# Kernel optimization log

Measured on AMD Instinct MI355X. Metric: run time of the kernel, lower is better.

## Reference

```python
import jax, jax.numpy as jnp
import numpy as np

C = 16          # in_channels // 4
EXP = 16        # expand_rate
SHIFTS = [1, 3, 5, 7]
BN_EPS = 1e-5

# fixed directional-difference kernels (non-trainable in the torch module)
_tmp1 = np.array([[[-1,0,0],[0,1,0],[0,0,0]],
                  [[0,-1,0],[0,1,0],[0,0,0]],
                  [[0,0,-1],[0,1,0],[0,0,0]],
                  [[0,0,0],[-1,1,0],[0,0,0]]], dtype=np.float32).reshape(4,1,3,3)
_tmp2 = _tmp1[:, :, ::-1, ::-1].copy()
K1 = jnp.asarray(np.tile(np.concatenate([_tmp1, _tmp2], 0), (C,1,1,1)))  # [8C,1,3,3]
K2 = jnp.asarray(np.tile(np.concatenate([_tmp2, _tmp1], 0), (C,1,1,1)))  # [8C,1,3,3]

def conv(x, w, groups=1, dilation=1, bias=None):
    out = jax.lax.conv_general_dilated(
        x, w, window_strides=(1,1), padding='SAME',
        rhs_dilation=(dilation, dilation),
        dimension_numbers=('NCHW','OIHW','NCHW'),
        feature_group_count=groups)
    if bias is not None:
        out = out + bias[None, :, None, None]
    return out

def setup_inputs() -> dict:
    key = jax.random.key(0)
    ks = jax.random.split(key, 20)
    B, Cin, H, W = 4, 64, 256, 256
    inp = {
        'cen': jax.random.normal(ks[0], (B, Cin, H, W), jnp.float32),
        'mas': jax.random.normal(ks[1], (B, 1, H, W), jnp.float32),
        'w_in': jax.random.normal(ks[2], (C, Cin, 1, 1), jnp.float32) * 0.1,
        'b_in': jax.random.normal(ks[3], (C,), jnp.float32) * 0.1,
        'w_c0': jax.random.normal(ks[4], (C, C, 1, 1), jnp.float32) * 0.1,
        'b_c0': jax.random.normal(ks[5], (C,), jnp.float32) * 0.1,
        'w_c1': jax.random.normal(ks[6], (C, C, 3, 3), jnp.float32) * 0.1,
        'b_c1': jax.random.normal(ks[7], (C,), jnp.float32) * 0.1,
        'w_c2': jax.random.normal(ks[8], (C, C, 5, 5), jnp.float32) * 0.05,
        'b_c2': jax.random.normal(ks[9], (C,), jnp.float32) * 0.1,
        'w_c3': jax.random.normal(ks[10], (C, C, 7, 7), jnp.float32) * 0.05,
        'b_c3': jax.random.normal(ks[11], (C,), jnp.float32) * 0.1,
        'scales1': jax.random.normal(ks[12], (4,), jnp.float32) * 0.1,
        'scales2': jax.random.normal(ks[13], (C * EXP, 8, 1, 1), jnp.float32) * 0.1,
        'scales3': jax.random.normal(ks[14], (C, EXP, 1, 1), jnp.float32) * 0.1,
        'w_base': jax.random.normal(ks[15], (C, C, 3, 3), jnp.float32) * 0.1,
        'bn_gamma': jnp.ones((C,), jnp.float32),
        'bn_beta': jnp.zeros((C,), jnp.float32),
        'bn_mean': jnp.zeros((C,), jnp.float32),
        'bn_var': jnp.ones((C,), jnp.float32),
        'w_out': jax.random.normal(ks[16], (1, C, 1, 1), jnp.float32) * 0.1,
        'b_out': jax.random.normal(ks[17], (1,), jnp.float32) * 0.1,
    }
    return inp

def reference(cen, mas, w_in, b_in, w_c0, b_c0, w_c1, b_c1, w_c2, b_c2, w_c3, b_c3,
              scales1, scales2, scales3, w_base, bn_gamma, bn_beta, bn_mean, bn_var,
              w_out, b_out):
    x = conv(cen, w_in, bias=b_in)                      # [B,C,H,W]
    k3 = jax.nn.softmax(scales2, axis=1)                # [8C*2? no: [C*EXP,8,1,1]
    k4 = jax.nn.softmax(scales3, axis=1)                # [C,EXP,1,1]
    conv_ws = [(w_c0, b_c0), (w_c1, b_c1), (w_c2, b_c2), (w_c3, b_c3)]
    outs = []
    for (wc, bc), shift in zip(conv_ws, SHIFTS):
        c = conv(x, wc, bias=bc)                        # [B,C,H,W]
        o1 = conv(c, K1, groups=C, dilation=shift)      # [B,8C,H,W]
        o2 = conv(c, K2, groups=C, dilation=shift)
        o1 = conv(o1, k3, groups=C)                     # [B,C*EXP,H,W]
        o2 = conv(o2, k3, groups=C)
        o = jnp.sort(o1 * o2, axis=2)                   # sort along H
        o = jax.nn.silu(o)
        o = conv(o, k4, groups=C)                       # [B,C,H,W]
        outs.append(o)
    outs = jnp.stack(outs, axis=-1)                     # [B,C,H,W,4]
    outs = jnp.max(outs, axis=-1) + jnp.mean(outs, axis=-1)
    # out_conv = BaseConv(3x3 conv -> BN(eval) -> SiLU) then 1x1 conv to 1 ch
    h = conv(outs, w_base)
    h = (h - bn_mean[None, :, None, None]) * jax.lax.rsqrt(bn_var + BN_EPS)[None, :, None, None]
    h = h * bn_gamma[None, :, None, None] + bn_beta[None, :, None, None]
    h = jax.nn.silu(h)
    h = conv(h, w_out, bias=b_out)
    out_mask = jax.nn.sigmoid(h)                        # [B,1,H,W]
    s = jax.nn.softmax(scales1, axis=-1)
    m = jax.nn.sigmoid(mas)
    return cen * (out_mask * m * s[0] + m * s[1] + s[2] * out_mask + s[3])
```

## Files before the change

kernel.cpp:

```cpp
#include <hip/hip_runtime.h>

#define HW 65536

constexpr int OFF_X    = 0;
constexpr int OFF_CT   = 4194304;
constexpr int OFF_MAX  = 8388608;
constexpr int OFF_SUM  = 12582912;
constexpr int OFF_MASK = 16777216;
constexpr int P_K3  = 17039360;
constexpr int P_K3S = P_K3  + 2048;
constexpr int P_K4  = P_K3S + 2048;
constexpr int P_S1  = P_K4  + 256;
constexpr int P_BNS = P_S1  + 4;
constexpr int P_BNB = P_BNS + 16;
constexpr int P_WRI = P_BNB + 16;
constexpr int P_WR0 = P_WRI + 1024;
constexpr int P_WR1 = P_WR0 + 256;
constexpr int P_WR2 = P_WR1 + 2304;
constexpr int P_WR3 = P_WR2 + 6400;
constexpr int P_WRB = P_WR3 + 12544;
constexpr int P_K3H  = P_WRB + 2304;
constexpr int P_K3SH = P_K3H + 1024;

typedef _Float16 hv2 __attribute__((ext_vector_type(2)));

__device__ __forceinline__ int h2i(hv2 v) { return __builtin_bit_cast(int, v); }
__device__ __forceinline__ hv2 i2h(int v) { return __builtin_bit_cast(hv2, v); }

__device__ __forceinline__ hv2 pkrtz(float a, float b) {
  return __builtin_bit_cast(hv2, __builtin_amdgcn_cvt_pkrtz(a, b));
}

__device__ __forceinline__ hv2 pk_fma_n(hv2 a, hv2 b, hv2 c) {
#if __has_builtin(__builtin_elementwise_fma)
  return __builtin_elementwise_fma(a, b, c);
#else
  return a * b + c;
#endif
}

__device__ __forceinline__ hv2 pkmin(hv2 a, hv2 b) {
  hv2 d; asm("v_pk_min_f16 %0, %1, %2" : "=v"(d) : "v"(a), "v"(b)); return d;
}
__device__ __forceinline__ hv2 pkmax(hv2 a, hv2 b) {
  hv2 d; asm("v_pk_max_f16 %0, %1, %2" : "=v"(d) : "v"(a), "v"(b)); return d;
}
__device__ __forceinline__ hv2 pkmul(hv2 a, hv2 b) {
  hv2 d; asm("v_pk_mul_f16 %0, %1, %2" : "=v"(d) : "v"(a), "v"(b)); return d;
}
__device__ __forceinline__ hv2 pkfma(hv2 a, hv2 b, hv2 c) {
  hv2 d; asm("v_pk_fma_f16 %0, %1, %2, %3" : "=v"(d) : "v"(a), "v"(b), "v"(c)); return d;
}

__device__ __forceinline__ hv2 sel32(bool c, hv2 a, hv2 b) {
  return i2h(c ? h2i(a) : h2i(b));
}

template <int LMASK>
__device__ __forceinline__ int lane_xor_i(int x) {
  if constexpr (LMASK < 32) {
    return __builtin_amdgcn_ds_swizzle(x, (LMASK << 10) | 0x1F);
  } else {
    return __shfl_xor(x, LMASK, 64);
  }
}

__device__ __forceinline__ float sigmoid_fast(float x) {
  return __fdividef(1.0f, 1.0f + __expf(-x));
}

__global__ void k_prep(const float* __restrict__ w_in, const float* __restrict__ w_c0,
                       const float* __restrict__ w_c1, const float* __restrict__ w_c2,
                       const float* __restrict__ w_c3, const float* __restrict__ w_base,
                       const float* __restrict__ scales1, const float* __restrict__ scales2,
                       const float* __restrict__ scales3, const float* __restrict__ bn_gamma,
                       const float* __restrict__ bn_beta, const float* __restrict__ bn_mean,
                       const float* __restrict__ bn_var, float* __restrict__ ws) {
  int tid = threadIdx.x;
  {
    const float* srow = scales2 + tid * 8;
    float v[8]; float mx = -1e30f;
    for (int j = 0; j < 8; j++) { v[j] = srow[j]; mx = fmaxf(mx, v[j]); }
    float s = 0.f;
    for (int j = 0; j < 8; j++) { v[j] = __expf(v[j] - mx); s += v[j]; }
    float inv = 1.0f / s;
    for (int j = 0; j < 8; j++) ws[P_K3 + tid * 8 + j] = v[j] * inv;
    for (int j = 0; j < 8; j++) ws[P_K3S + tid * 8 + j] = v[(j + 4) & 7] * inv;
  }
  if (tid < 16) {
    const float* srow = scales3 + tid * 16;
    float v[16]; float mx = -1e30f;
    for (int e = 0; e < 16; e++) { v[e] = srow[e]; mx = fmaxf(mx, v[e]); }
    float s = 0.f;
    for (int e = 0; e < 16; e++) { v[e] = __expf(v[e] - mx); s += v[e]; }
    float inv = 1.0f / s;
    for (int e = 0; e < 16; e++) ws[P_K4 + tid * 16 + e] = v[e] * inv;
  }
  if (tid == 0) {
    float v[4]; float mx = -1e30f;
    for (int i = 0; i < 4; i++) { v[i] = scales1[i]; mx = fmaxf(mx, v[i]); }
    float s = 0.f;
    for (int i = 0; i < 4; i++) { v[i] = __expf(v[i] - mx); s += v[i]; }
    for (int i = 0; i < 4; i++) ws[P_S1 + i] = v[i] / s;
  }
  if (tid < 16) {
    float rs = rsqrtf(bn_var[tid] + 1e-5f);
    float sc = bn_gamma[tid] * rs;
    ws[P_BNS + tid] = sc;
    ws[P_BNB + tid] = bn_beta[tid] - bn_mean[tid] * sc;
  }
  for (int i = tid; i < 1024; i += 256) { int ci = i >> 4, co = i & 15; ws[P_WRI + i] = w_in[co * 64 + ci]; }
  {
    uint32_t* w0 = (uint32_t*)(ws + P_WR0);
    for (int i = tid; i < 128; i += 256) {
      int cp = i & 7, ci = i >> 3;
      hv2 wv;
      wv.x = (_Float16)w_c0[(2 * cp) * 16 + ci];
      wv.y = (_Float16)w_c0[(2 * cp + 1) * 16 + ci];
      w0[ci * 8 + cp] = __builtin_bit_cast(uint32_t, wv);
    }
    uint32_t* w1 = (uint32_t*)(ws + P_WR1);
    for (int i = tid; i < 1152; i += 256) {
      int cp = i & 7; int r = i >> 3; int kw = r % 3; r /= 3; int kh = r % 3; int ci = r / 3;
      hv2 wv;
      wv.x = (_Float16)w_c1[((2 * cp) * 16 + ci) * 9 + kh * 3 + kw];
      wv.y = (_Float16)w_c1[((2 * cp + 1) * 16 + ci) * 9 + kh * 3 + kw];
      w1[((ci * 3 + kh) * 3 + kw) * 8 + cp] = __builtin_bit_cast(uint32_t, wv);
    }
    uint32_t* w2 = (uint32_t*)(ws + P_WR2);
    for (int i = tid; i < 3200; i += 256) {
      int cp = i & 7; int r = i >> 3; int kw = r % 5; r /= 5; int kh = r % 5; int ci = r / 5;
      hv2 wv;
      wv.x = (_Float16)w_c2[((2 * cp) * 16 + ci) * 25 + kh * 5 + kw];
      wv.y = (_Float16)w_c2[((2 * cp + 1) * 16 + ci) * 25 + kh * 5 + kw];
      w2[((ci * 5 + kh) * 5 + kw) * 8 + cp] = __builtin_bit_cast(uint32_t, wv);
    }
    uint32_t* w3 = (uint32_t*)(ws + P_WR3);
    for (int i = tid; i < 6272; i += 256) {
      int cp = i & 7; int r = i >> 3; int kw = r % 7; r /= 7; int kh = r % 7; int ci = r / 7;
      hv2 wv;
      wv.x = (_Float16)w_c3[((2 * cp) * 16 + ci) * 49 + kh * 7 + kw];
      wv.y = (_Float16)w_c3[((2 * cp + 1) * 16 + ci) * 49 + kh * 7 + kw];
      w3[((ci * 7 + kh) * 7 + kw) * 8 + cp] = __builtin_bit_cast(uint32_t, wv);
    }
  }
  for (int i = tid; i < 2304; i += 256) {
    int co = i & 15; int r = i >> 4; int kh = r % 3; r /= 3; int kw = r % 3; int g = r / 3;
    ws[P_WRB + i] = w_base[((co * 16 + g) * 3 + kh) * 3 + kw];
  }
  __syncthreads();
  uint32_t* k3h  = (uint32_t*)(ws + P_K3H);
  uint32_t* k3sh = (uint32_t*)(ws + P_K3SH);
  for (int i = tid; i < 1024; i += 256) {
    int g = i >> 6, p = (i >> 3) & 7, j = i & 7;
    hv2 wv, wvs;
    wv.x  = (_Float16)ws[P_K3 + g * 128 + (2 * p) * 8 + j];
    wv.y  = (_Float16)ws[P_K3 + g * 128 + (2 * p + 1) * 8 + j];
    wvs.x = (_Float16)ws[P_K3S + g * 128 + (2 * p) * 8 + j];
    wvs.y = (_Float16)ws[P_K3S + g * 128 + (2 * p + 1) * 8 + j];
    k3h[i]  = __builtin_bit_cast(uint32_t, wv);
    k3sh[i] = __builtin_bit_cast(uint32_t, wvs);
  }
}

__global__ __launch_bounds__(256) void k_in(const float* __restrict__ cen,
                                            const float* __restrict__ b_in,
                                            const float* __restrict__ ws,
                                            float* __restrict__ xT) {
  __shared__ float ldst[16 * 16 * 17];
  int tid = threadIdx.x;
  int b = blockIdx.z;
  int hbase = blockIdx.y * 16, wbase = blockIdx.x * 16;
  int ty = tid >> 4, tx = tid & 15;
  const float* wri = ws + P_WRI;
  float acc[16];
#pragma unroll
  for (int co = 0; co < 16; co++) acc[co] = b_in[co];
  const float* cp = cen + b * 64 * HW + (hbase + ty) * 256 + wbase + tx;
#pragma unroll 4
  for (int ci = 0; ci < 64; ci++) {
    float v = cp[ci * HW];
#pragma unroll
    for (int co = 0; co < 16; co++) acc[co] = fmaf(wri[ci * 16 + co], v, acc[co]);
  }
#pragma unroll
  for (int co = 0; co < 16; co++) ldst[(co * 16 + tx) * 17 + ty] = acc[co];
  __syncthreads();
  int wy = tid >> 4, hx = tid & 15;
#pragma unroll
  for (int ci = 0; ci < 16; ci++) {
    xT[((b * 16 + ci) << 16) + (wbase + wy) * 256 + hbase + hx] =
        ldst[(ci * 16 + wy) * 17 + hx];
  }
}

template <int KS>
__global__ __launch_bounds__(256) void k_conv(const float* __restrict__ xT,
                                              const float* __restrict__ bias,
                                              const uint32_t* __restrict__ wrh,
                                              float* __restrict__ cT) {
  constexpr int P = KS / 2;
  const int tid = threadIdx.x;
  const int lane = tid & 63;
  const int wv = (blockIdx.x << 2) + (tid >> 6);
  const int hseg = wv & 3;
  const int w = (wv >> 2) & 255;
  const int b = wv >> 10;
  const int hbase = hseg << 6;
  const float* xb = xT + ((b * 16) << 16);

  hv2 acc[8];
#pragma unroll
  for (int cp = 0; cp < 8; cp++) {
    hv2 bv;
    bv.x = (_Float16)bias[2 * cp];
    bv.y = (_Float16)bias[2 * cp + 1];
    acc[cp] = bv;
  }

  for (int ci = 0; ci < 16; ci++) {
#pragma unroll
    for (int kw = 0; kw < KS; kw++) {
      const int wc = w + kw - P;
      if ((unsigned)wc >= 256u) continue;
      const float* col = xb + (ci << 16) + (wc << 8);
      const int h0 = hbase + lane - P;
      float v0 = ((unsigned)h0 < 256u) ? col[h0] : 0.0f;
      float v1 = 0.0f;
      if (P > 0) {
        const int h1 = hbase + 64 - P + lane;
        v1 = (lane < 2 * P && (unsigned)h1 < 256u) ? col[h1] : 0.0f;
      }
#pragma unroll
      for (int kh = 0; kh < KS; kh++) {
        float tv;
        if (P == 0) {
          tv = v0;
        } else {
          const int s = lane + kh;
          float t0 = __shfl(v0, s & 63, 64);
          float t1 = __shfl(v1, (s - 64) & 63, 64);
          tv = (s < 64) ? t0 : t1;
        }
        const hv2 tp = pkrtz(tv, tv);
        const uint32_t* wp = wrh + ((ci * KS + kh) * KS + kw) * 8;
#pragma unroll
        for (int cp = 0; cp < 8; cp++)
          acc[cp] = pk_fma_n(i2h((int)wp[cp]), tp, acc[cp]);
      }
    }
  }
  float* o = cT + ((b * 16) << 16) + (w << 8) + hbase + lane;
#pragma unroll
  for (int cp = 0; cp < 8; cp++) {
    o[(2 * cp) << 16] = (float)acc[cp].x;
    o[(2 * cp + 1) << 16] = (float)acc[cp].y;
  }
}

__device__ __forceinline__ void ce_pair_h(hv2& a, hv2& b, bool up) {
  hv2 lo = pkmin(a, b);
  hv2 hi = pkmax(a, b);
  a = sel32(up, lo, hi);
  b = sel32(up, hi, lo);
}

template <int SIZE, int DIST>
__device__ __forceinline__ void stage_x_h(hv2 v[4], int i0) {
  const bool keepmin = (((i0 & DIST) == 0) == ((i0 & SIZE) == 0));
#pragma unroll
  for (int r = 0; r < 4; r++) {
    hv2 pv = i2h(lane_xor_i<(DIST >> 2)>(h2i(v[r])));
    v[r] = sel32(keepmin, pkmin(v[r], pv), pkmax(v[r], pv));
  }
}

template <int SIZE>
__device__ __forceinline__ void stage_d21_h(hv2 v[4], int i0) {
  bool up = ((i0 & SIZE) == 0);
  ce_pair_h(v[0], v[2], up); ce_pair_h(v[1], v[3], up);
  ce_pair_h(v[0], v[1], up); ce_pair_h(v[2], v[3], up);
}

__device__ __forceinline__ void sort256h(hv2 v[4], int lane) {
  int i0 = lane << 2;
  ce_pair_h(v[0], v[1], true); ce_pair_h(v[2], v[3], false);
  stage_d21_h<4>(v, i0);
  stage_x_h<8, 4>(v, i0); stage_d21_h<8>(v, i0);
  stage_x_h<16, 8>(v, i0); stage_x_h<16, 4>(v, i0); stage_d21_h<16>(v, i0);
  stage_x_h<32, 16>(v, i0); stage_x_h<32, 8>(v, i0); stage_x_h<32, 4>(v, i0); stage_d21_h<32>(v, i0);
  stage_x_h<64, 32>(v, i0); stage_x_h<64, 16>(v, i0); stage_x_h<64, 8>(v, i0); stage_x_h<64, 4>(v, i0); stage_d21_h<64>(v, i0);
  stage_x_h<128, 64>(v, i0); stage_x_h<128, 32>(v, i0); stage_x_h<128, 16>(v, i0); stage_x_h<128, 8>(v, i0); stage_x_h<128, 4>(v, i0); stage_d21_h<128>(v, i0);
  stage_x_h<256, 128>(v, i0); stage_x_h<256, 64>(v, i0); stage_x_h<256, 32>(v, i0); stage_x_h<256, 16>(v, i0); stage_x_h<256, 8>(v, i0); stage_x_h<256, 4>(v, i0); stage_d21_h<256>(v, i0);
}

template <int DIL>
__global__ __launch_bounds__(256) void k_branch(const float* __restrict__ cT,
                                                const float* __restrict__ ws,
                                                float* __restrict__ maxb,
                                                float* __restrict__ sumb,
                                                int initFlag) {
  const int tid = threadIdx.x;
  const int lane = tid & 63;
  const int wid = __builtin_amdgcn_readfirstlane(tid >> 6);
  const int wv = (blockIdx.x << 2) + wid;
  const int w = wv & 255;
  const int g = (wv >> 8) & 15;
  const int b = wv >> 12;
  const float* base = cT + ((b * 16 + g) << 16);

  float vals[3][3][4];
#pragma unroll
  for (int wi = 0; wi < 3; ++wi) {
    const int wc = w + (wi - 1) * DIL;
    const bool wok = ((unsigned)wc < 256u);
    const float* col = base + (wok ? wc : 0) * 256;
#pragma unroll
    for (int si = 0; si < 3; ++si) {
#pragma unroll
      for (int r = 0; r < 4; ++r) {
        const int h = lane + (r << 6) + (si - 1) * DIL;
        const bool ok = wok && ((unsigned)h < 256u);
        vals[wi][si][r] = ok ? col[h] : 0.0f;
      }
    }
  }
  hv2 ddh[8][4];
#pragma unroll
  for (int r = 0; r < 4; ++r) {
    const float c0 = vals[1][1][r];
    float d0 = c0 - vals[0][0][r];
    float d1 = c0 - vals[1][0][r];
    float d2 = c0 - vals[2][0][r];
    float d3 = c0 - vals[0][1][r];
    float d4 = c0 - vals[2][2][r];
    float d5 = c0 - vals[1][2][r];
    float d6 = c0 - vals[0][2][r];
    float d7 = c0 - vals[2][1][r];
    ddh[0][r] = pkrtz(d0, d0);
    ddh[1][r] = pkrtz(d1, d1);
    ddh[2][r] = pkrtz(d2, d2);
    ddh[3][r] = pkrtz(d3, d3);
    ddh[4][r] = pkrtz(d4, d4);
    ddh[5][r] = pkrtz(d5, d5);
    ddh[6][r] = pkrtz(d6, d6);
    ddh[7][r] = pkrtz(d7, d7);
  }
  float out[4] = {0.f, 0.f, 0.f, 0.f};
  const uint32_t* k3h  = (const uint32_t*)(ws + P_K3H)  + g * 64;
  const uint32_t* k3sh = (const uint32_t*)(ws + P_K3SH) + g * 64;
  const float* k4p = ws + P_K4 + g * 16;
#pragma unroll 1
  for (int p = 0; p < 8; ++p) {
    hv2 t[4];
    hv2 wk3[8], wk3s[8];
#pragma unroll
    for (int j = 0; j < 8; ++j) {
      wk3[j]  = i2h((int)k3h[p * 8 + j]);
      wk3s[j] = i2h((int)k3sh[p * 8 + j]);
    }
#pragma unroll
    for (int r = 0; r < 4; ++r) {
      hv2 o1 = pkmul(wk3[0], ddh[0][r]);
      hv2 o2 = pkmul(wk3s[0], ddh[0][r]);
#pragma unroll
      for (int j = 1; j < 8; ++j) {
        o1 = pkfma(wk3[j], ddh[j][r], o1);
        o2 = pkfma(wk3s[j], ddh[j][r], o2);
      }
      t[r] = pkmul(o1, o2);
    }
    sort256h(t, lane);
    const float k4a = k4p[2 * p], k4b = k4p[2 * p + 1];
#pragma unroll
    for (int r = 0; r < 4; ++r) {
      const float va = (float)t[r].x;
      const float vb = (float)t[r].y;
      out[r] = fmaf(k4a, va * sigmoid_fast(va), out[r]);
      out[r] = fmaf(k4b, vb * sigmoid_fast(vb), out[r]);
    }
  }
  const int obase = (((b * 16 + g) << 8) + w) * 256 + (lane << 2);
  float4 o4 = make_float4(out[0], out[1], out[2], out[3]);
  float4* mp = (float4*)(maxb + obase);
  float4* sp = (float4*)(sumb + obase);
  if (initFlag) {
    *mp = o4;
    *sp = o4;
  } else {
    float4 m = *mp;
    m.x = fmaxf(m.x, o4.x); m.y = fmaxf(m.y, o4.y);
    m.z = fmaxf(m.z, o4.z); m.w = fmaxf(m.w, o4.w);
    *mp = m;
    float4 s = *sp;
    s.x += o4.x; s.y += o4.y; s.z += o4.z; s.w += o4.w;
    *sp = s;
  }
}

__global__ __launch_bounds__(256) void k_tail(const float* __restrict__ maxb,
                                              const float* __restrict__ sumb,
                                              const float* __restrict__ ws,
                                              float* __restrict__ mask,
                                              const float* __restrict__ w_out,
                                              const float* __restrict__ b_out) {
  __shared__ float lds[16 * 18 * 18];
  __shared__ float ldsm[256];
  int tid = threadIdx.x;
  int b = blockIdx.z;
  int wbase = blockIdx.x * 16, hbase = blockIdx.y * 16;
  const float* mb = maxb + (b * 16) * HW;
  const float* sb = sumb + (b * 16) * HW;
  for (int i = tid; i < 16 * 18 * 18; i += 256) {
    int g = i / 324; int r = i % 324; int xx = r / 18, yy = r % 18;
    int wq = wbase + xx - 1, hq = hbase + yy - 1;
    float v = 0.0f;
    if (wq >= 0 && wq < 256 && hq >= 0 && hq < 256) {
      int idx = g * HW + wq * 256 + hq;
      v = mb[idx] + 0.25f * sb[idx];
    }
    lds[i] = v;
  }
  __syncthreads();
  int xw = tid >> 4, yh = tid & 15;
  float acc[16] = {0.f, 0.f, 0.f, 0.f, 0.f, 0.f, 0.f, 0.f,
                   0.f, 0.f, 0.f, 0.f, 0.f, 0.f, 0.f, 0.f};
  for (int g = 0; g < 16; g++) {
#pragma unroll
    for (int kw = 0; kw < 3; kw++) {
#pragma unroll
      for (int kh = 0; kh < 3; kh++) {
        float v = lds[g * 324 + (xw + kw) * 18 + (yh + kh)];
        const float* wp = ws + P_WRB + ((g * 3 + kw) * 3 + kh) * 16;
#pragma unroll
        for (int co = 0; co < 16; co++) acc[co] = fmaf(wp[co], v, acc[co]);
      }
    }
  }
  float mo = b_out[0];
#pragma unroll
  for (int co = 0; co < 16; co++) {
    float z = acc[co] * ws[P_BNS + co] + ws[P_BNB + co];
    float sl = z * sigmoid_fast(z);
    mo = fmaf(w_out[co], sl, mo);
  }
  float mk = sigmoid_fast(mo);
  ldsm[yh * 16 + xw] = mk;
  __syncthreads();
  int yy = tid >> 4, xx = tid & 15;
  mask[b * HW + (hbase + yy) * 256 + wbase + xx] = ldsm[yy * 16 + xx];
}

__global__ __launch_bounds__(256) void k_final(const float* __restrict__ cen,
                                               const float* __restrict__ mas,
                                               const float* __restrict__ mask,
                                               const float* __restrict__ ws,
                                               float* __restrict__ out) {
  int q = blockIdx.x * 256 + threadIdx.x;
  int b = q >> 14;
  int off = (q & 16383) << 2;
  int cbase = blockIdx.y * 16;
  float s0 = ws[P_S1], s1 = ws[P_S1 + 1], s2 = ws[P_S1 + 2], s3 = ws[P_S1 + 3];
  const float4 mk4 = *(const float4*)(mask + b * HW + off);
  const float4 ms4 = *(const float4*)(mas + b * HW + off);
  float f[4];
  {
    float mks[4] = {mk4.x, mk4.y, mk4.z, mk4.w};
    float mss[4] = {ms4.x, ms4.y, ms4.z, ms4.w};
#pragma unroll
    for (int k = 0; k < 4; k++) {
      float m = sigmoid_fast(mss[k]);
      f[k] = mks[k] * m * s0 + m * s1 + s2 * mks[k] + s3;
    }
  }
#pragma unroll 4
  for (int ci = cbase; ci < cbase + 16; ci++) {
    const float4 c4 = *(const float4*)(cen + (b * 64 + ci) * HW + off);
    float4 o4;
    o4.x = c4.x * f[0]; o4.y = c4.y * f[1]; o4.z = c4.z * f[2]; o4.w = c4.w * f[3];
    *(float4*)(out + (b * 64 + ci) * HW + off) = o4;
  }
}

extern "C" void kernel_launch(void* const* d_in, const int* in_sizes, int n_in,
                              void* d_out, int out_size, void* d_ws, size_t ws_size,
                              hipStream_t stream) {
  (void)in_sizes; (void)n_in; (void)out_size; (void)ws_size;
  const float* cen = (const float*)d_in[0];
  const float* mas = (const float*)d_in[1];
  const float* w_in = (const float*)d_in[2];
  const float* b_in = (const float*)d_in[3];
  const float* w_c0 = (const float*)d_in[4];
  const float* b_c0 = (const float*)d_in[5];
  const float* w_c1 = (const float*)d_in[6];
  const float* b_c1 = (const float*)d_in[7];
  const float* w_c2 = (const float*)d_in[8];
  const float* b_c2 = (const float*)d_in[9];
  const float* w_c3 = (const float*)d_in[10];
  const float* b_c3 = (const float*)d_in[11];
  const float* scales1 = (const float*)d_in[12];
  const float* scales2 = (const float*)d_in[13];
  const float* scales3 = (const float*)d_in[14];
  const float* w_base = (const float*)d_in[15];
  const float* bn_gamma = (const float*)d_in[16];
  const float* bn_beta = (const float*)d_in[17];
  const float* bn_mean = (const float*)d_in[18];
  const float* bn_var = (const float*)d_in[19];
  const float* w_out = (const float*)d_in[20];
  const float* b_out = (const float*)d_in[21];
  float* ws = (float*)d_ws;
  float* out = (float*)d_out;

  float* xT = ws + OFF_X;
  float* cT = ws + OFF_CT;
  float* maxb = ws + OFF_MAX;
  float* sumb = ws + OFF_SUM;
  float* mask = ws + OFF_MASK;

  k_prep<<<1, 256, 0, stream>>>(w_in, w_c0, w_c1, w_c2, w_c3, w_base, scales1, scales2,
                                scales3, bn_gamma, bn_beta, bn_mean, bn_var, ws);
  k_in<<<dim3(16, 16, 4), 256, 0, stream>>>(cen, b_in, ws, xT);

  k_conv<1><<<1024, 256, 0, stream>>>(xT, b_c0, (const uint32_t*)(ws + P_WR0), cT);
  k_branch<1><<<4096, 256, 0, stream>>>(cT, ws, maxb, sumb, 1);
  k_conv<3><<<1024, 256, 0, stream>>>(xT, b_c1, (const uint32_t*)(ws + P_WR1), cT);
  k_branch<3><<<4096, 256, 0, stream>>>(cT, ws, maxb, sumb, 0);
  k_conv<5><<<1024, 256, 0, stream>>>(xT, b_c2, (const uint32_t*)(ws + P_WR2), cT);
  k_branch<5><<<4096, 256, 0, stream>>>(cT, ws, maxb, sumb, 0);
  k_conv<7><<<1024, 256, 0, stream>>>(xT, b_c3, (const uint32_t*)(ws + P_WR3), cT);
  k_branch<7><<<4096, 256, 0, stream>>>(cT, ws, maxb, sumb, 0);

  k_tail<<<dim3(16, 16, 4), 256, 0, stream>>>(maxb, sumb, ws, mask, w_out, b_out);
  k_final<<<dim3(256, 4), 256, 0, stream>>>(cen, mas, mask, ws, out);
}
```

Measured before the change: 923.4 us.

## Fuse final gating into tail kernel, use DPP for lane swaps, unroll conv loop

Merges k_final into k_tail: the tail now computes the gating factor per pixel and applies it to all 64 channels of cen for its 16x16 tile, so the mask buffer is never written to or read back from global memory and one launch is removed. Lane-xor shuffles for masks 1 and 2 now use DPP moves instead of ds_swizzle. The conv input-channel loop is unrolled by 2. The fused tail writes 64-byte row segments per channel, which coalesce less well than the old streaming layout, and each block now does 16 iterations of global traffic.

```diff
diff --git a/kernel.cpp b/kernel.cpp
--- a/kernel.cpp
+++ b/kernel.cpp
@@ -6,7 +6,6 @@
 constexpr int OFF_CT   = 4194304;
 constexpr int OFF_MAX  = 8388608;
 constexpr int OFF_SUM  = 12582912;
-constexpr int OFF_MASK = 16777216;
 constexpr int P_K3  = 17039360;
 constexpr int P_K3S = P_K3  + 2048;
 constexpr int P_K4  = P_K3S + 2048;
@@ -58,7 +57,11 @@
 
 template <int LMASK>
 __device__ __forceinline__ int lane_xor_i(int x) {
-  if constexpr (LMASK < 32) {
+  if constexpr (LMASK == 1) {
+    return __builtin_amdgcn_mov_dpp(x, 0xB1, 0xF, 0xF, true);
+  } else if constexpr (LMASK == 2) {
+    return __builtin_amdgcn_mov_dpp(x, 0x4E, 0xF, 0xF, true);
+  } else if constexpr (LMASK < 32) {
     return __builtin_amdgcn_ds_swizzle(x, (LMASK << 10) | 0x1F);
   } else {
     return __shfl_xor(x, LMASK, 64);
@@ -218,6 +221,7 @@
     acc[cp] = bv;
   }
 
+#pragma unroll 2
   for (int ci = 0; ci < 16; ci++) {
 #pragma unroll
     for (int kw = 0; kw < KS; kw++) {
@@ -401,11 +405,13 @@
 __global__ __launch_bounds__(256) void k_tail(const float* __restrict__ maxb,
                                               const float* __restrict__ sumb,
                                               const float* __restrict__ ws,
-                                              float* __restrict__ mask,
+                                              const float* __restrict__ cen,
+                                              const float* __restrict__ mas,
                                               const float* __restrict__ w_out,
-                                              const float* __restrict__ b_out) {
+                                              const float* __restrict__ b_out,
+                                              float* __restrict__ out) {
   __shared__ float lds[16 * 18 * 18];
-  __shared__ float ldsm[256];
+  __shared__ float ldsf[256];
   int tid = threadIdx.x;
   int b = blockIdx.z;
   int wbase = blockIdx.x * 16, hbase = blockIdx.y * 16;
@@ -445,40 +451,32 @@
     mo = fmaf(w_out[co], sl, mo);
   }
   float mk = sigmoid_fast(mo);
-  ldsm[yh * 16 + xw] = mk;
+  ldsf[yh * 16 + xw] = mk;
   __syncthreads();
-  int yy = tid >> 4, xx = tid & 15;
-  mask[b * HW + (hbase + yy) * 256 + wbase + xx] = ldsm[yy * 16 + xx];
-}
-
-__global__ __launch_bounds__(256) void k_final(const float* __restrict__ cen,
-                                               const float* __restrict__ mas,
-                                               const float* __restrict__ mask,
-                                               const float* __restrict__ ws,
-                                               float* __restrict__ out) {
-  int q = blockIdx.x * 256 + threadIdx.x;
-  int b = q >> 14;
-  int off = (q & 16383) << 2;
-  int cbase = blockIdx.y * 16;
-  float s0 = ws[P_S1], s1 = ws[P_S1 + 1], s2 = ws[P_S1 + 2], s3 = ws[P_S1 + 3];
-  const float4 mk4 = *(const float4*)(mask + b * HW + off);
-  const float4 ms4 = *(const float4*)(mas + b * HW + off);
-  float f[4];
   {
-    float mks[4] = {mk4.x, mk4.y, mk4.z, mk4.w};
-    float mss[4] = {ms4.x, ms4.y, ms4.z, ms4.w};
-#pragma unroll
-    for (int k = 0; k < 4; k++) {
-      float m = sigmoid_fast(mss[k]);
-      f[k] = mks[k] * m * s0 + m * s1 + s2 * mks[k] + s3;
-    }
-  }
+    int yy = tid >> 4, xx = tid & 15;
+    float mkv = ldsf[yy * 16 + xx];
+    float m = sigmoid_fast(mas[b * HW + (hbase + yy) * 256 + wbase + xx]);
+    float s0 = ws[P_S1], s1 = ws[P_S1 + 1], s2 = ws[P_S1 + 2], s3 = ws[P_S1 + 3];
+    float f = mkv * m * s0 + m * s1 + s2 * mkv + s3;
+    ldsf[yy * 16 + xx] = f;
+  }
+  __syncthreads();
+  const float* cb = cen + b * 64 * HW;
+  float* ob = out + b * 64 * HW;
 #pragma unroll 4
-  for (int ci = cbase; ci < cbase + 16; ci++) {
-    const float4 c4 = *(const float4*)(cen + (b * 64 + ci) * HW + off);
+  for (int it = 0; it < 16; ++it) {
+    int flat = it * 256 + tid;
+    int ci = flat >> 6;
+    int rr = flat & 63;
+    int yy = rr >> 2, wq = rr & 3;
+    const float* fr = &ldsf[yy * 16 + wq * 4];
+    float4 f4 = make_float4(fr[0], fr[1], fr[2], fr[3]);
+    int addr = ci * HW + (hbase + yy) * 256 + wbase + wq * 4;
+    const float4 c4 = *(const float4*)(cb + addr);
     float4 o4;
-    o4.x = c4.x * f[0]; o4.y = c4.y * f[1]; o4.z = c4.z * f[2]; o4.w = c4.w * f[3];
-    *(float4*)(out + (b * 64 + ci) * HW + off) = o4;
+    o4.x = c4.x * f4.x; o4.y = c4.y * f4.y; o4.z = c4.z * f4.z; o4.w = c4.w * f4.w;
+    *(float4*)(ob + addr) = o4;
   }
 }
 
@@ -515,7 +513,6 @@
   float* cT = ws + OFF_CT;
   float* maxb = ws + OFF_MAX;
   float* sumb = ws + OFF_SUM;
-  float* mask = ws + OFF_MASK;
 
   k_prep<<<1, 256, 0, stream>>>(w_in, w_c0, w_c1, w_c2, w_c3, w_base, scales1, scales2,
                                 scales3, bn_gamma, bn_beta, bn_mean, bn_var, ws);
@@ -530,6 +527,5 @@
   k_conv<7><<<1024, 256, 0, stream>>>(xT, b_c3, (const uint32_t*)(ws + P_WR3), cT);
   k_branch<7><<<4096, 256, 0, stream>>>(cT, ws, maxb, sumb, 0);
 
-  k_tail<<<dim3(16, 16, 4), 256, 0, stream>>>(maxb, sumb, ws, mask, w_out, b_out);
-  k_final<<<dim3(256, 4), 256, 0, stream>>>(cen, mas, mask, ws, out);
-}
+  k_tail<<<dim3(16, 16, 4), 256, 0, stream>>>(maxb, sumb, ws, cen, mas, w_out, b_out, out);
+}
```

Result: no change. 939.3 us (+1.7%).
